# Kernel optimization log

Measured on AMD Instinct MI355X. Metric: run time of the kernel, lower is better.

The kernel has to match this reference:

```python
import jax, jax.numpy as jnp
import numpy as np

N = 50000       # nodes
E = 800000      # nonzeros in sparse Laplacian (avg degree 16)
C_IN = 256
C_OUT = 128
NUM_CLASS = 7


def setup_inputs() -> dict:
    key = jax.random.key(0)
    ks = jax.random.split(key, 8)
    x = jax.random.normal(ks[0], (N, C_IN), jnp.float32)
    rows = jax.random.randint(ks[1], (E,), 0, N, jnp.int32)
    cols = jax.random.randint(ks[2], (E,), 0, N, jnp.int32)
    vals = jax.random.normal(ks[3], (E,), jnp.float32) * 0.1
    W_in = jax.random.normal(ks[4], (C_IN, C_OUT), jnp.float32) / np.sqrt(C_IN)
    b_in = jnp.zeros((C_OUT,), jnp.float32)
    delta = jnp.ones((1,), jnp.float32)
    a = jnp.ones((1,), jnp.float32)
    W_out = jax.random.normal(ks[5], (C_OUT, NUM_CLASS), jnp.float32) / np.sqrt(C_OUT)
    b_out = jnp.zeros((NUM_CLASS,), jnp.float32)
    return dict(x=x, vals=vals, W_in=W_in, b_in=b_in, delta=delta, a=a,
                W_out=W_out, b_out=b_out, rows=rows, cols=cols)


def spmm(rows, cols, vals, x):
    # sparse [N,N] @ dense [N,C] in COO form: out[r] += v * x[c]
    return jax.ops.segment_sum(vals[:, None] * x[cols], rows, num_segments=N)


def reference(x, vals, W_in, b_in, delta, a, W_out, b_out, rows, cols):
    # dropout is inactive in eval mode
    h = jnp.tanh(x @ W_in + b_in)                      # [N, C_OUT]
    Tx1 = spmm(rows, cols, vals, h)
    Tx2 = spmm(rows, cols, vals, Tx1)
    Tx3 = spmm(rows, cols, vals, Tx2)
    d = delta[0]
    av = a[0]
    low = Tx3 + (-3.0 * d - av) * Tx2 + (3.0 * d**2 + 2.0 * d * av) * Tx1 - (d**3 + d**2 * av) * h
    high = Tx3 + (-3.0 * d + av) * Tx2 + (3.0 * d**2 - 2.0 * d * av) * Tx1 + (d**2 * av - d**3) * h
    dn = jnp.linalg.norm(low - h, axis=1, keepdims=True)   # [N,1]
    high_delta = spmm(rows, cols, vals, dn)                # [N,1]
    normal = (high_delta - high_delta.min()) / (high_delta.max() - high_delta.min())
    final = (1.0 - normal) * low + normal * high
    y = jax.nn.relu(final) @ W_out + b_out                 # [N, NUM_CLASS]
    return jax.nn.log_softmax(y, axis=1)
```

## Files before the change

### kernel.cpp

```cpp
#include <hip/hip_runtime.h>
#include <hip/hip_bf16.h>
#include <float.h>
#include <math.h>

#define N_NODES 50000
#define CIN 256
#define COUT 128
#define NCLS 7

typedef unsigned short ushort_t;

static __device__ __forceinline__ float wave_sum(float v) {
#pragma unroll
  for (int off = 32; off > 0; off >>= 1) v += __shfl_xor(v, off, 64);
  return v;
}

static __device__ __forceinline__ unsigned enc_f(float f) {
  unsigned u = __float_as_uint(f);
  return (u & 0x80000000u) ? ~u : (u | 0x80000000u);
}
static __device__ __forceinline__ float dec_f(unsigned u) {
  return __uint_as_float((u & 0x80000000u) ? (u & 0x7FFFFFFFu) : ~u);
}

static __device__ __forceinline__ float bf2f(ushort_t u) {
  return __uint_as_float(((unsigned)u) << 16);
}
static __device__ __forceinline__ ushort_t f2bf(float f) {
  __hip_bfloat16 b = __float2bfloat16(f);
  return *reinterpret_cast<ushort_t*>(&b);
}


__global__ void hist_kernel(const int* __restrict__ rows, int* __restrict__ counts, int e) {
  int i = blockIdx.x * blockDim.x + threadIdx.x;
  if (i < e) atomicAdd(&counts[rows[i]], 1);
}

__global__ __launch_bounds__(256) void scan1_kernel(const int* __restrict__ counts,
                                                    int* __restrict__ rowptr,
                                                    int* __restrict__ bsum, int n) {
  __shared__ int sh[256];
  int t = threadIdx.x;
  int base = blockIdx.x * 1024 + t * 4;
  int v0 = (base + 0 < n) ? counts[base + 0] : 0;
  int v1 = (base + 1 < n) ? counts[base + 1] : 0;
  int v2 = (base + 2 < n) ? counts[base + 2] : 0;
  int v3 = (base + 3 < n) ? counts[base + 3] : 0;
  int s = v0 + v1 + v2 + v3;
  sh[t] = s;
  __syncthreads();
  for (int off = 1; off < 256; off <<= 1) {
    int add = (t >= off) ? sh[t - off] : 0;
    __syncthreads();
    sh[t] += add;
    __syncthreads();
  }
  int ex = sh[t] - s;
  if (base + 0 < n) rowptr[base + 0] = ex;
  ex += v0;
  if (base + 1 < n) rowptr[base + 1] = ex;
  ex += v1;
  if (base + 2 < n) rowptr[base + 2] = ex;
  ex += v2;
  if (base + 3 < n) rowptr[base + 3] = ex;
  if (t == 255) bsum[blockIdx.x] = sh[255];
}

__global__ void scan2_kernel(int* __restrict__ bsum, int nb) {
  int t = threadIdx.x;
  int v = (t < nb) ? bsum[t] : 0;
  int orig = v;
#pragma unroll
  for (int off = 1; off < 64; off <<= 1) {
    int u = __shfl_up(v, off, 64);
    if (t >= off) v += u;
  }
  if (t < nb) bsum[t] = v - orig;
}

__global__ void scan3_kernel(int* __restrict__ rowptr, int* __restrict__ cursor,
                             const int* __restrict__ bsum, unsigned* __restrict__ mnmx_u,
                             int n, int e) {
  int i = blockIdx.x * blockDim.x + threadIdx.x;
  if (i < n) {
    int v = rowptr[i] + bsum[i >> 10];
    rowptr[i] = v;
    cursor[i] = v;
  }
  if (i == 0) {
    rowptr[n] = e;
    mnmx_u[0] = 0xFFFFFFFFu;
    mnmx_u[1] = 0u;
  }
}

__global__ void scatter_kernel(const int* __restrict__ rows, const int* __restrict__ cols,
                               const float* __restrict__ vals, int* __restrict__ cursor,
                               int* __restrict__ colv, float* __restrict__ valv, int e) {
  int i = blockIdx.x * blockDim.x + threadIdx.x;
  if (i < e) {
    int r = rows[i];
    int idx = atomicAdd(&cursor[r], 1);
    colv[idx] = cols[i];
    valv[idx] = vals[i];
  }
}

__global__ __launch_bounds__(256) void gemm_tanh_kernel(const float* __restrict__ x,
                                                        const float* __restrict__ W,
                                                        const float* __restrict__ b,
                                                        float* __restrict__ h,
                                                        ushort_t* __restrict__ h_bf, int n) {
  __shared__ float xs[16][36];
  __shared__ float wsh[16][COUT];
  int t = threadIdx.x;
  int block_row = blockIdx.x * 32;
  int tc = t & 31, tr = t >> 5;
  int c0 = tc * 4, r0 = tr * 4;
  float acc[4][4] = {};
  int lr = t >> 3;
  int lk = (t & 7) * 2;
  int grow = block_row + lr;
  bool rvalid = grow < n;
  const float* xrow = x + (size_t)(rvalid ? grow : 0) * CIN;
  int wr = t >> 4;
  int wc = (t & 15) * 8;

  for (int k0 = 0; k0 < CIN; k0 += 16) {
    float2 xv = rvalid ? *(const float2*)(xrow + k0 + lk) : make_float2(0.f, 0.f);
    xs[lk][lr] = xv.x;
    xs[lk + 1][lr] = xv.y;
    const float* wp = W + (size_t)(k0 + wr) * COUT + wc;
    float4 w0 = *(const float4*)wp;
    float4 w1 = *(const float4*)(wp + 4);
    *(float4*)&wsh[wr][wc] = w0;
    *(float4*)&wsh[wr][wc + 4] = w1;
    __syncthreads();
#pragma unroll
    for (int kk = 0; kk < 16; ++kk) {
      float4 xa = *(const float4*)&xs[kk][r0];
      float4 wv = *(const float4*)&wsh[kk][c0];
      float xr[4] = {xa.x, xa.y, xa.z, xa.w};
      float wvv[4] = {wv.x, wv.y, wv.z, wv.w};
#pragma unroll
      for (int i = 0; i < 4; ++i)
#pragma unroll
        for (int j = 0; j < 4; ++j) acc[i][j] = fmaf(xr[i], wvv[j], acc[i][j]);
    }
    __syncthreads();
  }
  float4 bv = *(const float4*)(b + c0);
  float bb[4] = {bv.x, bv.y, bv.z, bv.w};
#pragma unroll
  for (int i = 0; i < 4; ++i) {
    int row = block_row + r0 + i;
    if (row < n) {
      float4 o;
      o.x = tanhf(acc[i][0] + bb[0]);
      o.y = tanhf(acc[i][1] + bb[1]);
      o.z = tanhf(acc[i][2] + bb[2]);
      o.w = tanhf(acc[i][3] + bb[3]);
      *(float4*)&h[(size_t)row * COUT + c0] = o;
      ushort4 ub;
      ub.x = f2bf(o.x); ub.y = f2bf(o.y); ub.z = f2bf(o.z); ub.w = f2bf(o.w);
      *(ushort4*)&h_bf[(size_t)row * COUT + c0] = ub;
    }
  }
}

static __device__ __forceinline__ float4 spmm_row_bf(const int* __restrict__ rowptr,
                                                     const int* __restrict__ colv,
                                                     const float* __restrict__ valv,
                                                     const ushort_t* __restrict__ xin_bf,
                                                     int r, int c) {
  int s = rowptr[r], e = rowptr[r + 1];
  float4 acc = make_float4(0.f, 0.f, 0.f, 0.f);
  int i = s;
  for (; i + 4 <= e; i += 4) {
    int k0 = colv[i], k1 = colv[i + 1], k2 = colv[i + 2], k3 = colv[i + 3];
    float v0 = valv[i], v1 = valv[i + 1], v2 = valv[i + 2], v3 = valv[i + 3];
    ushort4 u0 = *(const ushort4*)&xin_bf[(size_t)k0 * COUT + c];
    ushort4 u1 = *(const ushort4*)&xin_bf[(size_t)k1 * COUT + c];
    ushort4 u2 = *(const ushort4*)&xin_bf[(size_t)k2 * COUT + c];
    ushort4 u3 = *(const ushort4*)&xin_bf[(size_t)k3 * COUT + c];
    acc.x = fmaf(v0, bf2f(u0.x), acc.x); acc.y = fmaf(v0, bf2f(u0.y), acc.y);
    acc.z = fmaf(v0, bf2f(u0.z), acc.z); acc.w = fmaf(v0, bf2f(u0.w), acc.w);
    acc.x = fmaf(v1, bf2f(u1.x), acc.x); acc.y = fmaf(v1, bf2f(u1.y), acc.y);
    acc.z = fmaf(v1, bf2f(u1.z), acc.z); acc.w = fmaf(v1, bf2f(u1.w), acc.w);
    acc.x = fmaf(v2, bf2f(u2.x), acc.x); acc.y = fmaf(v2, bf2f(u2.y), acc.y);
    acc.z = fmaf(v2, bf2f(u2.z), acc.z); acc.w = fmaf(v2, bf2f(u2.w), acc.w);
    acc.x = fmaf(v3, bf2f(u3.x), acc.x); acc.y = fmaf(v3, bf2f(u3.y), acc.y);
    acc.z = fmaf(v3, bf2f(u3.z), acc.z); acc.w = fmaf(v3, bf2f(u3.w), acc.w);
  }
  for (; i < e; ++i) {
    int k = colv[i];
    float v = valv[i];
    ushort4 u = *(const ushort4*)&xin_bf[(size_t)k * COUT + c];
    acc.x = fmaf(v, bf2f(u.x), acc.x); acc.y = fmaf(v, bf2f(u.y), acc.y);
    acc.z = fmaf(v, bf2f(u.z), acc.z); acc.w = fmaf(v, bf2f(u.w), acc.w);
  }
  return acc;
}

__global__ __launch_bounds__(256) void spmm_dense_kernel(const int* __restrict__ rowptr,
                                                         const int* __restrict__ colv,
                                                         const float* __restrict__ valv,
                                                         const ushort_t* __restrict__ xin_bf,
                                                         float* __restrict__ xout,
                                                         ushort_t* __restrict__ xout_bf, int n) {
  int r = blockIdx.x * 8 + (threadIdx.x >> 5);
  if (r >= n) return;
  int c = (threadIdx.x & 31) * 4;
  float4 acc = spmm_row_bf(rowptr, colv, valv, xin_bf, r, c);
  *(float4*)&xout[(size_t)r * COUT + c] = acc;
  ushort4 ub;
  ub.x = f2bf(acc.x); ub.y = f2bf(acc.y); ub.z = f2bf(acc.z); ub.w = f2bf(acc.w);
  *(ushort4*)&xout_bf[(size_t)r * COUT + c] = ub;
}

__global__ __launch_bounds__(256) void spmm_dense_dn_kernel(const int* __restrict__ rowptr,
                                                            const int* __restrict__ colv,
                                                            const float* __restrict__ valv,
                                                            const ushort_t* __restrict__ t2_bf,
                                                            const float* __restrict__ t2,
                                                            float* __restrict__ t3out,
                                                            const float* __restrict__ h,
                                                            const float* __restrict__ t1,
                                                            const float* __restrict__ delta,
                                                            const float* __restrict__ a_s,
                                                            float* __restrict__ dn, int n) {
  int r = blockIdx.x * 8 + (threadIdx.x >> 5);
  if (r >= n) return;
  int c = (threadIdx.x & 31) * 4;
  float4 acc = spmm_row_bf(rowptr, colv, valv, t2_bf, r, c);
  size_t idx = (size_t)r * COUT + c;
  *(float4*)&t3out[idx] = acc;

  float d = delta[0], av = a_s[0];
  float cl2 = -3.f * d - av;
  float cl1 = 3.f * d * d + 2.f * d * av;
  float cl0 = -(d * d * d + d * d * av);
  float4 hv = *(const float4*)&h[idx];
  float4 v1 = *(const float4*)&t1[idx];
  float4 v2 = *(const float4*)&t2[idx];
  float dx = acc.x + cl2 * v2.x + cl1 * v1.x + cl0 * hv.x - hv.x;
  float dy = acc.y + cl2 * v2.y + cl1 * v1.y + cl0 * hv.y - hv.y;
  float dz = acc.z + cl2 * v2.z + cl1 * v1.z + cl0 * hv.z - hv.z;
  float dw = acc.w + cl2 * v2.w + cl1 * v1.w + cl0 * hv.w - hv.w;
  float ss = dx * dx + dy * dy + dz * dz + dw * dw;
#pragma unroll
  for (int off = 16; off > 0; off >>= 1) ss += __shfl_xor(ss, off, 64);
  if ((threadIdx.x & 31) == 0) dn[r] = sqrtf(ss);
}

__global__ __launch_bounds__(256) void spmm_vec_kernel(const int* __restrict__ rowptr,
                                                       const int* __restrict__ colv,
                                                       const float* __restrict__ valv,
                                                       const float* __restrict__ dn,
                                                       float* __restrict__ hd,
                                                       unsigned* __restrict__ mnmx_u, int n) {
  int r = blockIdx.x * blockDim.x + threadIdx.x;
  float acc = 0.f;
  bool valid = r < n;
  if (valid) {
    int s = rowptr[r], e = rowptr[r + 1];
    int i = s;
    float a0 = 0.f, a1 = 0.f, a2 = 0.f, a3 = 0.f;
    for (; i + 4 <= e; i += 4) {
      int k0 = colv[i], k1 = colv[i + 1], k2 = colv[i + 2], k3 = colv[i + 3];
      float v0 = valv[i], v1 = valv[i + 1], v2 = valv[i + 2], v3 = valv[i + 3];
      a0 = fmaf(v0, dn[k0], a0);
      a1 = fmaf(v1, dn[k1], a1);
      a2 = fmaf(v2, dn[k2], a2);
      a3 = fmaf(v3, dn[k3], a3);
    }
    acc = (a0 + a1) + (a2 + a3);
    for (; i < e; ++i) acc = fmaf(valv[i], dn[colv[i]], acc);
    hd[r] = acc;
  }
  float mn = valid ? acc : FLT_MAX;
  float mx = valid ? acc : -FLT_MAX;
#pragma unroll
  for (int off = 32; off > 0; off >>= 1) {
    mn = fminf(mn, __shfl_xor(mn, off, 64));
    mx = fmaxf(mx, __shfl_xor(mx, off, 64));
  }
  __shared__ float smn[4], smx[4];
  int w = threadIdx.x >> 6;
  if ((threadIdx.x & 63) == 0) { smn[w] = mn; smx[w] = mx; }
  __syncthreads();
  if (threadIdx.x == 0) {
    mn = fminf(fminf(smn[0], smn[1]), fminf(smn[2], smn[3]));
    mx = fmaxf(fmaxf(smx[0], smx[1]), fmaxf(smx[2], smx[3]));
    atomicMin(&mnmx_u[0], enc_f(mn));
    atomicMax(&mnmx_u[1], enc_f(mx));
  }
}

__global__ __launch_bounds__(256) void final_kernel(const float* __restrict__ h,
                                                    const float* __restrict__ t1,
                                                    const float* __restrict__ t2,
                                                    const float* __restrict__ t3,
                                                    const float* __restrict__ hd,
                                                    const unsigned* __restrict__ mnmx_u,
                                                    const float* __restrict__ delta,
                                                    const float* __restrict__ a_s,
                                                    const float* __restrict__ W_out,
                                                    const float* __restrict__ b_out,
                                                    float* __restrict__ out, int n) {
  __shared__ float wsh[COUT * NCLS];
  __shared__ float bsh[NCLS];
  for (int i = threadIdx.x; i < COUT * NCLS; i += 256) wsh[i] = W_out[i];
  if (threadIdx.x < NCLS) bsh[threadIdx.x] = b_out[threadIdx.x];
  __syncthreads();
  int w = threadIdx.x >> 6;
  int lane = threadIdx.x & 63;
  int r = blockIdx.x * 4 + w;
  if (r >= n) return;
  float d = delta[0], av = a_s[0];
  float cl2 = -3.f * d - av;
  float cl1 = 3.f * d * d + 2.f * d * av;
  float cl0 = -(d * d * d + d * d * av);
  float ch2 = -3.f * d + av;
  float ch1 = 3.f * d * d - 2.f * d * av;
  float ch0 = d * d * av - d * d * d;
  float mn = dec_f(mnmx_u[0]), mx = dec_f(mnmx_u[1]);
  float normal = (hd[r] - mn) / (mx - mn);
  float onemn = 1.f - normal;
  size_t base = (size_t)r * COUT;
  float f[2];
#pragma unroll
  for (int p = 0; p < 2; ++p) {
    int c = lane + p * 64;
    size_t idx = base + c;
    float hv = h[idx], v1 = t1[idx], v2 = t2[idx], v3 = t3[idx];
    float low = v3 + cl2 * v2 + cl1 * v1 + cl0 * hv;
    float high = v3 + ch2 * v2 + ch1 * v1 + ch0 * hv;
    float fin = onemn * low + normal * high;
    f[p] = fmaxf(fin, 0.f);
  }
  float y[NCLS];
#pragma unroll
  for (int j = 0; j < NCLS; ++j) {
    float pv = f[0] * wsh[lane * NCLS + j] + f[1] * wsh[(lane + 64) * NCLS + j];
    y[j] = wave_sum(pv) + bsh[j];
  }
  if (lane == 0) {
    float m = y[0];
#pragma unroll
    for (int j = 1; j < NCLS; ++j) m = fmaxf(m, y[j]);
    float s = 0.f;
#pragma unroll
    for (int j = 0; j < NCLS; ++j) s += expf(y[j] - m);
    float lse = m + logf(s);
#pragma unroll
    for (int j = 0; j < NCLS; ++j) out[(size_t)r * NCLS + j] = y[j] - lse;
  }
}

extern "C" void kernel_launch(void* const* d_in, const int* in_sizes, int n_in,
                              void* d_out, int out_size, void* d_ws, size_t ws_size,
                              hipStream_t stream) {
  (void)n_in; (void)out_size; (void)ws_size;
  const float* x     = (const float*)d_in[0];
  const float* vals  = (const float*)d_in[1];
  const float* W_in  = (const float*)d_in[2];
  const float* b_in  = (const float*)d_in[3];
  const float* delta = (const float*)d_in[4];
  const float* a_in  = (const float*)d_in[5];
  const float* W_out = (const float*)d_in[6];
  const float* b_out = (const float*)d_in[7];
  const int* rows    = (const int*)d_in[8];
  const int* cols    = (const int*)d_in[9];
  float* out = (float*)d_out;
  const int n = N_NODES;
  const int e = in_sizes[1];

  char* p = (char*)d_ws;
  auto alloc = [&](size_t bytes) {
    char* r = p;
    p += (bytes + 255) & ~(size_t)255;
    return r;
  };
  float* h   = (float*)alloc((size_t)n * COUT * 4);
  float* t1  = (float*)alloc((size_t)n * COUT * 4);
  float* t2  = (float*)alloc((size_t)n * COUT * 4);
  float* t3  = (float*)alloc((size_t)n * COUT * 4);
  ushort_t* h_bf  = (ushort_t*)alloc((size_t)n * COUT * 2);
  ushort_t* t1_bf = (ushort_t*)alloc((size_t)n * COUT * 2);
  ushort_t* t2_bf = (ushort_t*)alloc((size_t)n * COUT * 2);
  float* dn = (float*)alloc((size_t)n * 4);
  float* hd = (float*)alloc((size_t)n * 4);
  int* rowptr = (int*)alloc((size_t)(n + 1) * 4);
  int* cursor = (int*)alloc((size_t)n * 4);
  int* colv   = (int*)alloc((size_t)e * 4);
  float* valv = (float*)alloc((size_t)e * 4);
  int* bsum   = (int*)alloc(64 * 4);
  unsigned* mnmx_u = (unsigned*)alloc(2 * 4);

  hipMemsetAsync(cursor, 0, (size_t)n * 4, stream);
  hist_kernel<<<(e + 255) / 256, 256, 0, stream>>>(rows, cursor, e);
  const int nb = (n + 1023) / 1024;
  scan1_kernel<<<nb, 256, 0, stream>>>(cursor, rowptr, bsum, n);
  scan2_kernel<<<1, 64, 0, stream>>>(bsum, nb);
  scan3_kernel<<<(n + 255) / 256, 256, 0, stream>>>(rowptr, cursor, bsum, mnmx_u, n, e);
  scatter_kernel<<<(e + 255) / 256, 256, 0, stream>>>(rows, cols, vals, cursor, colv, valv, e);

  gemm_tanh_kernel<<<(n + 31) / 32, 256, 0, stream>>>(x, W_in, b_in, h, h_bf, n);

  spmm_dense_kernel<<<(n + 7) / 8, 256, 0, stream>>>(rowptr, colv, valv, h_bf, t1, t1_bf, n);
  spmm_dense_kernel<<<(n + 7) / 8, 256, 0, stream>>>(rowptr, colv, valv, t1_bf, t2, t2_bf, n);
  spmm_dense_dn_kernel<<<(n + 7) / 8, 256, 0, stream>>>(rowptr, colv, valv, t2_bf, t2, t3,
                                                        h, t1, delta, a_in, dn, n);

  spmm_vec_kernel<<<(n + 255) / 256, 256, 0, stream>>>(rowptr, colv, valv, dn, hd, mnmx_u, n);

  final_kernel<<<(n + 3) / 4, 256, 0, stream>>>(h, t1, t2, t3, hd, mnmx_u, delta, a_in,
                                                W_out, b_out, out, n);
}
```

Measured before the change: 397.5 us.

## Use bf16 MFMA for input GEMM with pre-transposed bf16 weights

Replaces the fp32 FMA tiled GEMM computing tanh(x@W_in+b) with a matrix-core kernel using mfma_f32_16x16x32_bf16. A small extra kernel converts W_in to a transposed bf16 layout first, and x is converted to bf16 while being staged in shared memory. This aims to cut the compute cost of the 50000x256x128 GEMM but lowers input precision to bf16 and adds one launch. The epilogue now writes scalar rather than vector stores.

```diff
diff --git a/kernel.cpp b/kernel.cpp
--- a/kernel.cpp
+++ b/kernel.cpp
@@ -9,6 +9,8 @@
 #define NCLS 7
 
 typedef unsigned short ushort_t;
+typedef __attribute__((ext_vector_type(8))) short bf16x8;
+typedef __attribute__((ext_vector_type(4))) float f32x4;
 
 static __device__ __forceinline__ float wave_sum(float v) {
 #pragma unroll
@@ -108,64 +110,81 @@
   }
 }
 
-__global__ __launch_bounds__(256) void gemm_tanh_kernel(const float* __restrict__ x,
-                                                        const float* __restrict__ W,
-                                                        const float* __restrict__ b,
-                                                        float* __restrict__ h,
-                                                        ushort_t* __restrict__ h_bf, int n) {
-  __shared__ float xs[16][36];
-  __shared__ float wsh[16][COUT];
+__global__ void wtrans_kernel(const float* __restrict__ W, ushort_t* __restrict__ W_T) {
+  int i = blockIdx.x * 256 + threadIdx.x;
+  int k = i >> 7, c = i & 127;
+  W_T[(size_t)c * CIN + k] = f2bf(W[i]);
+}
+
+__global__ __launch_bounds__(256) void gemm_tanh_mfma_kernel(const float* __restrict__ x,
+                                                             const ushort_t* __restrict__ W_T,
+                                                             const float* __restrict__ bias,
+                                                             float* __restrict__ h,
+                                                             ushort_t* __restrict__ h_bf, int n) {
+  __shared__ short xs[32][72];
+  __shared__ short wsT[128][72];
   int t = threadIdx.x;
+  int lane = t & 63;
+  int w = t >> 6;
   int block_row = blockIdx.x * 32;
-  int tc = t & 31, tr = t >> 5;
-  int c0 = tc * 4, r0 = tr * 4;
-  float acc[4][4] = {};
-  int lr = t >> 3;
-  int lk = (t & 7) * 2;
-  int grow = block_row + lr;
-  bool rvalid = grow < n;
-  const float* xrow = x + (size_t)(rvalid ? grow : 0) * CIN;
-  int wr = t >> 4;
-  int wc = (t & 15) * 8;
-
-  for (int k0 = 0; k0 < CIN; k0 += 16) {
-    float2 xv = rvalid ? *(const float2*)(xrow + k0 + lk) : make_float2(0.f, 0.f);
-    xs[lk][lr] = xv.x;
-    xs[lk + 1][lr] = xv.y;
-    const float* wp = W + (size_t)(k0 + wr) * COUT + wc;
-    float4 w0 = *(const float4*)wp;
-    float4 w1 = *(const float4*)(wp + 4);
-    *(float4*)&wsh[wr][wc] = w0;
-    *(float4*)&wsh[wr][wc + 4] = w1;
-    __syncthreads();
-#pragma unroll
-    for (int kk = 0; kk < 16; ++kk) {
-      float4 xa = *(const float4*)&xs[kk][r0];
-      float4 wv = *(const float4*)&wsh[kk][c0];
-      float xr[4] = {xa.x, xa.y, xa.z, xa.w};
-      float wvv[4] = {wv.x, wv.y, wv.z, wv.w};
-#pragma unroll
-      for (int i = 0; i < 4; ++i)
-#pragma unroll
-        for (int j = 0; j < 4; ++j) acc[i][j] = fmaf(xr[i], wvv[j], acc[i][j]);
+  int rw = (w & 1) * 16;
+  int cg = (w >> 1) * 64;
+
+  int xr = t >> 3;
+  int xk = (t & 7) * 8;
+  int grow_s = block_row + xr;
+  bool rvalid = grow_s < n;
+  const float* xrow = x + (size_t)(rvalid ? grow_s : 0) * CIN;
+  int wcol = t >> 1;
+  int wk = (t & 1) * 32;
+  const ushort_t* wtrow = W_T + (size_t)wcol * CIN;
+
+  f32x4 acc[4];
+#pragma unroll
+  for (int c = 0; c < 4; ++c) acc[c] = (f32x4){0.f, 0.f, 0.f, 0.f};
+
+  for (int k0 = 0; k0 < CIN; k0 += 64) {
+    float4 a0 = rvalid ? *(const float4*)(xrow + k0 + xk) : make_float4(0.f, 0.f, 0.f, 0.f);
+    float4 a1 = rvalid ? *(const float4*)(xrow + k0 + xk + 4) : make_float4(0.f, 0.f, 0.f, 0.f);
+    bf16x8 xb;
+    xb[0] = (short)f2bf(a0.x); xb[1] = (short)f2bf(a0.y);
+    xb[2] = (short)f2bf(a0.z); xb[3] = (short)f2bf(a0.w);
+    xb[4] = (short)f2bf(a1.x); xb[5] = (short)f2bf(a1.y);
+    xb[6] = (short)f2bf(a1.z); xb[7] = (short)f2bf(a1.w);
+    *(bf16x8*)&xs[xr][xk] = xb;
+#pragma unroll
+    for (int j = 0; j < 4; ++j) {
+      bf16x8 wv = *(const bf16x8*)(wtrow + k0 + wk + j * 8);
+      *(bf16x8*)&wsT[wcol][wk + j * 8] = wv;
     }
     __syncthreads();
-  }
-  float4 bv = *(const float4*)(b + c0);
-  float bb[4] = {bv.x, bv.y, bv.z, bv.w};
-#pragma unroll
-  for (int i = 0; i < 4; ++i) {
-    int row = block_row + r0 + i;
-    if (row < n) {
-      float4 o;
-      o.x = tanhf(acc[i][0] + bb[0]);
-      o.y = tanhf(acc[i][1] + bb[1]);
-      o.z = tanhf(acc[i][2] + bb[2]);
-      o.w = tanhf(acc[i][3] + bb[3]);
-      *(float4*)&h[(size_t)row * COUT + c0] = o;
-      ushort4 ub;
-      ub.x = f2bf(o.x); ub.y = f2bf(o.y); ub.z = f2bf(o.z); ub.w = f2bf(o.w);
-      *(ushort4*)&h_bf[(size_t)row * COUT + c0] = ub;
+    int ar = rw + (lane & 15);
+    int koff = (lane >> 4) * 8;
+    bf16x8 fa0 = *(const bf16x8*)&xs[ar][koff];
+    bf16x8 fa1 = *(const bf16x8*)&xs[ar][32 + koff];
+#pragma unroll
+    for (int c = 0; c < 4; ++c) {
+      int bc = cg + c * 16 + (lane & 15);
+      bf16x8 fb0 = *(const bf16x8*)&wsT[bc][koff];
+      bf16x8 fb1 = *(const bf16x8*)&wsT[bc][32 + koff];
+      acc[c] = __builtin_amdgcn_mfma_f32_16x16x32_bf16(fa0, fb0, acc[c], 0, 0, 0);
+      acc[c] = __builtin_amdgcn_mfma_f32_16x16x32_bf16(fa1, fb1, acc[c], 0, 0, 0);
+    }
+    __syncthreads();
+  }
+  int rbase = block_row + rw + (lane >> 4) * 4;
+#pragma unroll
+  for (int c = 0; c < 4; ++c) {
+    int colg = cg + c * 16 + (lane & 15);
+    float bv = bias[colg];
+#pragma unroll
+    for (int m = 0; m < 4; ++m) {
+      int row = rbase + m;
+      if (row < n) {
+        float v = tanhf(acc[c][m] + bv);
+        h[(size_t)row * COUT + colg] = v;
+        h_bf[(size_t)row * COUT + colg] = f2bf(v);
+      }
     }
   }
 }
@@ -391,6 +410,7 @@
   ushort_t* h_bf  = (ushort_t*)alloc((size_t)n * COUT * 2);
   ushort_t* t1_bf = (ushort_t*)alloc((size_t)n * COUT * 2);
   ushort_t* t2_bf = (ushort_t*)alloc((size_t)n * COUT * 2);
+  ushort_t* W_T   = (ushort_t*)alloc((size_t)CIN * COUT * 2);
   float* dn = (float*)alloc((size_t)n * 4);
   float* hd = (float*)alloc((size_t)n * 4);
   int* rowptr = (int*)alloc((size_t)(n + 1) * 4);
@@ -408,7 +428,8 @@
   scan3_kernel<<<(n + 255) / 256, 256, 0, stream>>>(rowptr, cursor, bsum, mnmx_u, n, e);
   scatter_kernel<<<(e + 255) / 256, 256, 0, stream>>>(rows, cols, vals, cursor, colv, valv, e);
 
-  gemm_tanh_kernel<<<(n + 31) / 32, 256, 0, stream>>>(x, W_in, b_in, h, h_bf, n);
+  wtrans_kernel<<<(CIN * COUT + 255) / 256, 256, 0, stream>>>(W_in, W_T);
+  gemm_tanh_mfma_kernel<<<(n + 31) / 32, 256, 0, stream>>>(x, W_T, b_in, h, h_bf, n);
 
   spmm_dense_kernel<<<(n + 7) / 8, 256, 0, stream>>>(rowptr, colv, valv, h_bf, t1, t1_bf, n);
   spmm_dense_kernel<<<(n + 7) / 8, 256, 0, stream>>>(rowptr, colv, valv, t1_bf, t2, t2_bf, n);
```

Result: faster. 374.0 us (-5.9%).
